# Kernel optimization log

Hardware: AMD Instinct MI355X
Metric: run time of the kernel (lower is better)

## Reference

```python
import jax, jax.numpy as jnp
import numpy as np

N_PATCHES = 16
HID = 8
HEADS = 2
DH = HID // HEADS          # 4
L = 2                       # n_blocks
DIM = 10                    # betas.shape[0]
C = 3
S_DIM = 224
PS = S_DIM // N_PATCHES     # 14
INPUT_D = C * PS * PS       # 588
SEQ = N_PATCHES ** 2 + 1    # 257
MLP = 4 * HID               # 32
EPS = 1e-5


def _pos_embed():
    i = np.arange(SEQ, dtype=np.float64)[:, None]
    j = np.arange(HID, dtype=np.float64)[None, :]
    ang = i / 10000.0 ** ((j - (j % 2)) / HID)
    pe = np.where(j % 2 == 0, np.sin(ang), np.cos(ang))
    return jnp.asarray(pe, jnp.float32)


def setup_inputs() -> dict:
    key = jax.random.key(0)
    ks = jax.random.split(key, 24)
    g = lambda k, shape: (jax.random.normal(k, shape, jnp.float32) * 0.1)
    inp = {
        'images': jax.random.normal(ks[0], (512, C, S_DIM, S_DIM), jnp.float32),
        'inputs_labels': jax.random.randint(ks[1], (512,), 0, C),
        'Wm': g(ks[2], (INPUT_D, HID)), 'bm': g(ks[3], (HID,)),
        'cls_table': g(ks[4], (C, HID)),
        'pe': _pos_embed(),
        'ln1_g': jnp.ones((L, HID)), 'ln1_b': jnp.zeros((L, HID)),
        'Wq': g(ks[5], (L, HEADS, DH, DH)), 'bq': g(ks[6], (L, HEADS, DH)),
        'Wk': g(ks[7], (L, HEADS, DH, DH)), 'bk': g(ks[8], (L, HEADS, DH)),
        'Wv': g(ks[9], (L, HEADS, DH, DH)), 'bv': g(ks[10], (L, HEADS, DH)),
        'ln2_g': jnp.ones((L, HID)), 'ln2_b': jnp.zeros((L, HID)),
        'W1': g(ks[11], (L, HID, MLP)), 'b1': g(ks[12], (L, MLP)),
        'W2': g(ks[13], (L, MLP, HID)), 'b2': g(ks[14], (L, HID)),
        'Wf': g(ks[15], (HID, DIM)), 'bf': g(ks[16], (DIM,)),
    }
    return inp


def _layernorm(x, g, b):
    m = jnp.mean(x, axis=-1, keepdims=True)
    v = jnp.mean(jnp.square(x - m), axis=-1, keepdims=True)
    return (x - m) * jax.lax.rsqrt(v + EPS) * g + b


def _forward(images, inputs_labels, Wm, bm, cls_table, pe,
             ln1_g, ln1_b, Wq, bq, Wk, bk, Wv, bv,
             ln2_g, ln2_b, W1, b1, W2, b2, Wf, bf):
    n = images.shape[0]
    # patchify: [n,C,H,W] -> [n, n_patches^2, C*ps*ps]
    p = images.reshape(n, C, N_PATCHES, PS, N_PATCHES, PS)
    p = p.transpose(0, 2, 4, 1, 3, 5).reshape(n, N_PATCHES ** 2, INPUT_D)
    tokens = p @ Wm + bm                                # [n, 256, HID]
    cls = cls_table[inputs_labels][:, None, :]          # [n, 1, HID]
    x = jnp.concatenate([cls, tokens], axis=1) + pe[None]  # [n, SEQ, HID]
    scale = 1.0 / jnp.sqrt(jnp.float32(DH))
    for l in range(L):
        h = _layernorm(x, ln1_g[l], ln1_b[l]).reshape(n, SEQ, HEADS, DH)
        q = jnp.einsum('nshd,hde->nhse', h, Wq[l]) + bq[l][None, :, None, :]
        k = jnp.einsum('nshd,hde->nhse', h, Wk[l]) + bk[l][None, :, None, :]
        v = jnp.einsum('nshd,hde->nhse', h, Wv[l]) + bv[l][None, :, None, :]
        att = jax.nn.softmax(jnp.einsum('nhse,nhte->nhst', q, k) * scale, axis=-1)
        o = jnp.einsum('nhst,nhte->nhse', att, v)       # [n,H,S,DH]
        x = x + o.transpose(0, 2, 1, 3).reshape(n, SEQ, HID)
        h2 = _layernorm(x, ln2_g[l], ln2_b[l])
        x = x + jax.nn.gelu(h2 @ W1[l] + b1[l], approximate=False) @ W2[l] + b2[l]
    return x[:, 0] @ Wf + bf                            # [n, DIM]


def reference(images, inputs_labels, Wm, bm, cls_table, pe,
              ln1_g, ln1_b, Wq, bq, Wk, bk, Wv, bv,
              ln2_g, ln2_b, W1, b1, W2, b2, Wf, bf):
    return _forward(images, inputs_labels, Wm, bm, cls_table, pe,
                    ln1_g, ln1_b, Wq, bq, Wk, bk, Wv, bv,
                    ln2_g, ln2_b, W1, b1, W2, b2, Wf, bf)
```

## Files before the change

kernel.cpp:

```cpp
#include <hip/hip_runtime.h>

#define N_IMG_D 150528
#define CH_STRIDE 50176

__global__ __launch_bounds__(256) void k_patch_embed(
    const float* __restrict__ img, const float* __restrict__ Wm,
    const float* __restrict__ bm, const float* __restrict__ pe,
    float* __restrict__ xws)
{
    __shared__ __align__(16) float wmA[588 * 4];
    __shared__ __align__(16) float wmB[588 * 4];
    __shared__ __align__(16) float red[224 * 8];

    const int t = threadIdx.x;
    const int b = blockIdx.x;
    const int n = b >> 4, py = b & 15;

    for (int i = t; i < 1176; i += 256) {
        float4 w = reinterpret_cast<const float4*>(Wm)[i];
        float* dst = (i & 1) ? wmB : wmA;
        *reinterpret_cast<float4*>(dst + (i >> 1) * 4) = w;
    }
    __syncthreads();

    if (t < 224) {
        const int rp = t / 112;
        const int t1 = t - rp * 112;
        const int px = t1 / 7;
        const int j  = t1 - px * 7;
        const int col0 = 2 * j;
        const float* ib = img + (size_t)n * N_IMG_D + (py * 14) * 224 + px * 14 + col0;
        float a0=0,a1=0,a2=0,a3=0,a4=0,a5=0,a6=0,a7=0;
        int c = 0, r = rp;
        const float* wA = wmA + (rp * 14 + col0) * 4;
        const float* wB = wmB + (rp * 14 + col0) * 4;
        #pragma unroll
        for (int it = 0; it < 21; ++it) {
            const float2 v = *reinterpret_cast<const float2*>(ib + c * CH_STRIDE + r * 224);
            const float4 wa0 = *reinterpret_cast<const float4*>(wA);
            const float4 wa1 = *reinterpret_cast<const float4*>(wA + 4);
            const float4 wb0 = *reinterpret_cast<const float4*>(wB);
            const float4 wb1 = *reinterpret_cast<const float4*>(wB + 4);
            a0 += v.x * wa0.x + v.y * wa1.x;
            a1 += v.x * wa0.y + v.y * wa1.y;
            a2 += v.x * wa0.z + v.y * wa1.z;
            a3 += v.x * wa0.w + v.y * wa1.w;
            a4 += v.x * wb0.x + v.y * wb1.x;
            a5 += v.x * wb0.y + v.y * wb1.y;
            a6 += v.x * wb0.z + v.y * wb1.z;
            a7 += v.x * wb0.w + v.y * wb1.w;
            r += 2;
            if (r >= 14) { r -= 14; c += 1; }
            wA += 28 * 4; wB += 28 * 4;
        }
        *reinterpret_cast<float4*>(red + t * 8)     = make_float4(a0, a1, a2, a3);
        *reinterpret_cast<float4*>(red + t * 8 + 4) = make_float4(a4, a5, a6, a7);
    }
    __syncthreads();

    if (t < 128) {
        const int px = t >> 3, e = t & 7;
        float s = 0.f;
        #pragma unroll
        for (int rp = 0; rp < 2; ++rp) {
            #pragma unroll
            for (int j = 0; j < 7; ++j)
                s += red[(rp * 112 + px * 7 + j) * 8 + e];
        }
        const int row = 1 + py * 16 + px;
        s += bm[e] + pe[row * 8 + e];
        xws[((size_t)n * 257 + row) * 8 + e] = s;
    }
}

__global__ __launch_bounds__(576) void k_transformer(
    const float* __restrict__ xws, const int* __restrict__ labels,
    const float* __restrict__ cls_table, const float* __restrict__ pe,
    const float* __restrict__ ln1_g, const float* __restrict__ ln1_b,
    const float* __restrict__ Wq, const float* __restrict__ bq,
    const float* __restrict__ Wk, const float* __restrict__ bk,
    const float* __restrict__ Wv, const float* __restrict__ bv,
    const float* __restrict__ ln2_g, const float* __restrict__ ln2_b,
    const float* __restrict__ W1, const float* __restrict__ b1,
    const float* __restrict__ W2, const float* __restrict__ b2,
    const float* __restrict__ Wf, const float* __restrict__ bf,
    float* __restrict__ out)
{
    __shared__ __align__(16) float xb[257 * 9];
    __shared__ __align__(16) float hb[257 * 9];
    __shared__ __align__(16) float kb[2 * 257 * 4];
    __shared__ __align__(16) float vb[2 * 257 * 4];
    __shared__ float wqs[64], wks[64], wvs[64];
    __shared__ float bqs[16], bks[16], bvs[16];
    __shared__ float w1s[512], b1s[64], w2s[512], b2s[16];

    const int t = threadIdx.x;
    const int n = blockIdx.x;
    const float* xn = xws + (size_t)n * 2056;

    for (int i = t; i < 64; i += 576) { wqs[i] = Wq[i]; wks[i] = Wk[i]; wvs[i] = Wv[i]; b1s[i] = b1[i]; }
    for (int i = t; i < 16; i += 576) { bqs[i] = bq[i]; bks[i] = bk[i]; bvs[i] = bv[i]; b2s[i] = b2[i]; }
    for (int i = t; i < 512; i += 576) { w1s[i] = W1[i]; w2s[i] = W2[i]; }

    if (t < 512) {
        float4 v = reinterpret_cast<const float4*>(xn)[t + 2];
        const int s = (t + 2) >> 1;
        const int e0 = (t & 1) ? 4 : 0;
        float* d = xb + s * 9 + e0;
        d[0] = v.x; d[1] = v.y; d[2] = v.z; d[3] = v.w;
    } else if (t < 520) {
        const int e = t - 512;
        xb[e] = cls_table[labels[n] * 8 + e] + pe[e];
    }
    __syncthreads();

    for (int l = 0; l < 2; ++l) {
        if (t < 257) {
            float v0[8]; float m = 0.f;
            #pragma unroll
            for (int e = 0; e < 8; ++e) { v0[e] = xb[t * 9 + e]; m += v0[e]; }
            m *= 0.125f;
            float var = 0.f;
            #pragma unroll
            for (int e = 0; e < 8; ++e) { float d = v0[e] - m; var += d * d; }
            var *= 0.125f;
            const float rs = rsqrtf(var + 1e-5f);
            const float* g = ln1_g + l * 8; const float* bb = ln1_b + l * 8;
            #pragma unroll
            for (int e = 0; e < 8; ++e) hb[t * 9 + e] = (v0[e] - m) * rs * g[e] + bb[e];
        }
        __syncthreads();

        if (t < 514) {
            const int h = (t >= 257) ? 1 : 0;
            const int s = t - 257 * h;
            float hv[4];
            #pragma unroll
            for (int d = 0; d < 4; ++d) hv[d] = hb[s * 9 + h * 4 + d];
            const float* wk = wks + (l * 2 + h) * 16; const float* bk_ = bks + (l * 2 + h) * 4;
            const float* wv = wvs + (l * 2 + h) * 16; const float* bv_ = bvs + (l * 2 + h) * 4;
            float kk[4], vv[4];
            #pragma unroll
            for (int e = 0; e < 4; ++e) { kk[e] = bk_[e]; vv[e] = bv_[e]; }
            #pragma unroll
            for (int d = 0; d < 4; ++d)
                #pragma unroll
                for (int e = 0; e < 4; ++e) {
                    kk[e] += hv[d] * wk[d * 4 + e];
                    vv[e] += hv[d] * wv[d * 4 + e];
                }
            *reinterpret_cast<float4*>(kb + (h * 257 + s) * 4) = make_float4(kk[0], kk[1], kk[2], kk[3]);
            *reinterpret_cast<float4*>(vb + (h * 257 + s) * 4) = make_float4(vv[0], vv[1], vv[2], vv[3]);
        }
        __syncthreads();

        if (t < 514) {
            const int h = (t >= 257) ? 1 : 0;
            const int s = t - 257 * h;
            float hv[4];
            #pragma unroll
            for (int d = 0; d < 4; ++d) hv[d] = hb[s * 9 + h * 4 + d];
            const float* wq = wqs + (l * 2 + h) * 16; const float* bq_ = bqs + (l * 2 + h) * 4;
            float q[4];
            #pragma unroll
            for (int e = 0; e < 4; ++e) q[e] = bq_[e];
            #pragma unroll
            for (int d = 0; d < 4; ++d)
                #pragma unroll
                for (int e = 0; e < 4; ++e) q[e] += hv[d] * wq[d * 4 + e];
            const float SC = 0.72134752044f;
            #pragma unroll
            for (int e = 0; e < 4; ++e) q[e] *= SC;

            const float4* kp = reinterpret_cast<const float4*>(kb) + h * 257;
            const float4* vp = reinterpret_cast<const float4*>(vb) + h * 257;
            float lsum = 0.f, o0 = 0.f, o1 = 0.f, o2 = 0.f, o3 = 0.f;
            #pragma unroll 4
            for (int tt = 0; tt < 257; ++tt) {
                const float4 kk = kp[tt];
                const float s2 = q[0] * kk.x + q[1] * kk.y + q[2] * kk.z + q[3] * kk.w;
                const float p = exp2f(s2);
                lsum += p;
                const float4 vv = vp[tt];
                o0 += p * vv.x; o1 += p * vv.y; o2 += p * vv.z; o3 += p * vv.w;
            }
            const float inv = 1.0f / lsum;
            float* xr = xb + s * 9 + h * 4;
            xr[0] += o0 * inv; xr[1] += o1 * inv; xr[2] += o2 * inv; xr[3] += o3 * inv;
        }
        __syncthreads();

        if (t < 257) {
            float v0[8]; float m = 0.f;
            #pragma unroll
            for (int e = 0; e < 8; ++e) { v0[e] = xb[t * 9 + e]; m += v0[e]; }
            m *= 0.125f;
            float var = 0.f;
            #pragma unroll
            for (int e = 0; e < 8; ++e) { float d = v0[e] - m; var += d * d; }
            var *= 0.125f;
            const float rs = rsqrtf(var + 1e-5f);
            const float* g = ln2_g + l * 8; const float* bb = ln2_b + l * 8;
            #pragma unroll
            for (int e = 0; e < 8; ++e) hb[t * 9 + e] = (v0[e] - m) * rs * g[e] + bb[e];
        }
        __syncthreads();

        if (t < 257) {
            float hv[8];
            #pragma unroll
            for (int e = 0; e < 8; ++e) hv[e] = hb[t * 9 + e];
            float acc[8] = {0.f, 0.f, 0.f, 0.f, 0.f, 0.f, 0.f, 0.f};
            const float* w1 = w1s + l * 256; const float* bb1 = b1s + l * 32;
            const float* w2 = w2s + l * 256; const float* bb2 = b2s + l * 8;
            for (int u = 0; u < 32; ++u) {
                float a = bb1[u];
                #pragma unroll
                for (int e = 0; e < 8; ++e) a += hv[e] * w1[e * 32 + u];
                const float gl = 0.5f * a * (1.0f + erff(a * 0.70710678f));
                #pragma unroll
                for (int e = 0; e < 8; ++e) acc[e] += gl * w2[u * 8 + e];
            }
            #pragma unroll
            for (int e = 0; e < 8; ++e) xb[t * 9 + e] += acc[e] + bb2[e];
        }
        __syncthreads();
    }

    if (t < 10) {
        float a = bf[t];
        #pragma unroll
        for (int e = 0; e < 8; ++e) a += xb[e] * Wf[e * 10 + t];
        out[(size_t)n * 10 + t] = a;
    }
}

extern "C" void kernel_launch(void* const* d_in, const int* in_sizes, int n_in,
                              void* d_out, int out_size, void* d_ws, size_t ws_size,
                              hipStream_t stream) {
    const float* img    = (const float*)d_in[0];
    const int*   labels = (const int*)  d_in[1];
    const float* Wm     = (const float*)d_in[2];
    const float* bm     = (const float*)d_in[3];
    const float* cls    = (const float*)d_in[4];
    const float* pe     = (const float*)d_in[5];
    const float* ln1_g  = (const float*)d_in[6];
    const float* ln1_b  = (const float*)d_in[7];
    const float* Wq     = (const float*)d_in[8];
    const float* bq     = (const float*)d_in[9];
    const float* Wk     = (const float*)d_in[10];
    const float* bk     = (const float*)d_in[11];
    const float* Wv     = (const float*)d_in[12];
    const float* bv     = (const float*)d_in[13];
    const float* ln2_g  = (const float*)d_in[14];
    const float* ln2_b  = (const float*)d_in[15];
    const float* W1     = (const float*)d_in[16];
    const float* b1     = (const float*)d_in[17];
    const float* W2     = (const float*)d_in[18];
    const float* b2     = (const float*)d_in[19];
    const float* Wf     = (const float*)d_in[20];
    const float* bf     = (const float*)d_in[21];
    float* out = (float*)d_out;
    float* xws = (float*)d_ws;

    const int n = in_sizes[0] / N_IMG_D;
    k_patch_embed<<<n * 16, 256, 0, stream>>>(img, Wm, bm, pe, xws);
    k_transformer<<<n, 576, 0, stream>>>(xws, labels, cls, pe, ln1_g, ln1_b,
        Wq, bq, Wk, bk, Wv, bv, ln2_g, ln2_b, W1, b1, W2, b2, Wf, bf, out);
}
```

Baseline: 538.6 us.

## Fuse LN1 with QKV projection and process two queries per attention thread

LayerNorm1 now computes Q, K and V for both heads directly in registers and writes them to shared memory. This removes the separate hb round trip and one barrier. The attention loop then gives each thread two query rows, so every K/V shared-memory load is reused twice, and only 258 threads are active instead of 514. In exchange, fewer waves run during attention, which is the dominant phase, so latency hiding may drop. A qb buffer is also added to shared memory.

```diff
diff --git a/kernel.cpp b/kernel.cpp
--- a/kernel.cpp
+++ b/kernel.cpp
@@ -88,6 +88,7 @@
 {
     __shared__ __align__(16) float xb[257 * 9];
     __shared__ __align__(16) float hb[257 * 9];
+    __shared__ __align__(16) float qb[2 * 257 * 4];
     __shared__ __align__(16) float kb[2 * 257 * 4];
     __shared__ __align__(16) float vb[2 * 257 * 4];
     __shared__ float wqs[64], wks[64], wvs[64];
@@ -114,6 +115,8 @@
     }
     __syncthreads();
 
+    const float SC = 0.72134752044f;
+
     for (int l = 0; l < 2; ++l) {
         if (t < 257) {
             float v0[8]; float m = 0.f;
@@ -126,67 +129,72 @@
             var *= 0.125f;
             const float rs = rsqrtf(var + 1e-5f);
             const float* g = ln1_g + l * 8; const float* bb = ln1_b + l * 8;
-            #pragma unroll
-            for (int e = 0; e < 8; ++e) hb[t * 9 + e] = (v0[e] - m) * rs * g[e] + bb[e];
-        }
-        __syncthreads();
-
-        if (t < 514) {
-            const int h = (t >= 257) ? 1 : 0;
-            const int s = t - 257 * h;
-            float hv[4];
-            #pragma unroll
-            for (int d = 0; d < 4; ++d) hv[d] = hb[s * 9 + h * 4 + d];
-            const float* wk = wks + (l * 2 + h) * 16; const float* bk_ = bks + (l * 2 + h) * 4;
-            const float* wv = wvs + (l * 2 + h) * 16; const float* bv_ = bvs + (l * 2 + h) * 4;
-            float kk[4], vv[4];
-            #pragma unroll
-            for (int e = 0; e < 4; ++e) { kk[e] = bk_[e]; vv[e] = bv_[e]; }
-            #pragma unroll
-            for (int d = 0; d < 4; ++d)
-                #pragma unroll
-                for (int e = 0; e < 4; ++e) {
-                    kk[e] += hv[d] * wk[d * 4 + e];
-                    vv[e] += hv[d] * wv[d * 4 + e];
+            float ln[8];
+            #pragma unroll
+            for (int e = 0; e < 8; ++e) ln[e] = (v0[e] - m) * rs * g[e] + bb[e];
+
+            #pragma unroll
+            for (int h = 0; h < 2; ++h) {
+                const int wb_ = (l * 2 + h);
+                const float* wq = wqs + wb_ * 16; const float* bq_ = bqs + wb_ * 4;
+                const float* wk = wks + wb_ * 16; const float* bk_ = bks + wb_ * 4;
+                const float* wv = wvs + wb_ * 16; const float* bv_ = bvs + wb_ * 4;
+                float qq[4], kk[4], vv[4];
+                #pragma unroll
+                for (int e = 0; e < 4; ++e) { qq[e] = bq_[e]; kk[e] = bk_[e]; vv[e] = bv_[e]; }
+                #pragma unroll
+                for (int d = 0; d < 4; ++d) {
+                    const float hd = ln[h * 4 + d];
+                    #pragma unroll
+                    for (int e = 0; e < 4; ++e) {
+                        qq[e] += hd * wq[d * 4 + e];
+                        kk[e] += hd * wk[d * 4 + e];
+                        vv[e] += hd * wv[d * 4 + e];
+                    }
                 }
-            *reinterpret_cast<float4*>(kb + (h * 257 + s) * 4) = make_float4(kk[0], kk[1], kk[2], kk[3]);
-            *reinterpret_cast<float4*>(vb + (h * 257 + s) * 4) = make_float4(vv[0], vv[1], vv[2], vv[3]);
-        }
-        __syncthreads();
-
-        if (t < 514) {
-            const int h = (t >= 257) ? 1 : 0;
-            const int s = t - 257 * h;
-            float hv[4];
-            #pragma unroll
-            for (int d = 0; d < 4; ++d) hv[d] = hb[s * 9 + h * 4 + d];
-            const float* wq = wqs + (l * 2 + h) * 16; const float* bq_ = bqs + (l * 2 + h) * 4;
-            float q[4];
-            #pragma unroll
-            for (int e = 0; e < 4; ++e) q[e] = bq_[e];
-            #pragma unroll
-            for (int d = 0; d < 4; ++d)
-                #pragma unroll
-                for (int e = 0; e < 4; ++e) q[e] += hv[d] * wq[d * 4 + e];
-            const float SC = 0.72134752044f;
-            #pragma unroll
-            for (int e = 0; e < 4; ++e) q[e] *= SC;
-
+                const int ri = (h * 257 + t) * 4;
+                *reinterpret_cast<float4*>(qb + ri) =
+                    make_float4(qq[0] * SC, qq[1] * SC, qq[2] * SC, qq[3] * SC);
+                *reinterpret_cast<float4*>(kb + ri) = make_float4(kk[0], kk[1], kk[2], kk[3]);
+                *reinterpret_cast<float4*>(vb + ri) = make_float4(vv[0], vv[1], vv[2], vv[3]);
+            }
+        }
+        __syncthreads();
+
+        if (t < 258) {
+            const int h = (t >= 129) ? 1 : 0;
+            const int j = t - 129 * h;
+            const int s0 = j;
+            const int s1 = j + 129;
+            const bool has2 = (j < 128);
+            const float4* qp = reinterpret_cast<const float4*>(qb) + h * 257;
             const float4* kp = reinterpret_cast<const float4*>(kb) + h * 257;
             const float4* vp = reinterpret_cast<const float4*>(vb) + h * 257;
-            float lsum = 0.f, o0 = 0.f, o1 = 0.f, o2 = 0.f, o3 = 0.f;
+            const float4 q0 = qp[s0];
+            const float4 q1 = qp[has2 ? s1 : s0];
+
+            float l0 = 0.f, o00 = 0.f, o01 = 0.f, o02 = 0.f, o03 = 0.f;
+            float l1 = 0.f, o10 = 0.f, o11 = 0.f, o12 = 0.f, o13 = 0.f;
             #pragma unroll 4
             for (int tt = 0; tt < 257; ++tt) {
                 const float4 kk = kp[tt];
-                const float s2 = q[0] * kk.x + q[1] * kk.y + q[2] * kk.z + q[3] * kk.w;
-                const float p = exp2f(s2);
-                lsum += p;
                 const float4 vv = vp[tt];
-                o0 += p * vv.x; o1 += p * vv.y; o2 += p * vv.z; o3 += p * vv.w;
-            }
-            const float inv = 1.0f / lsum;
-            float* xr = xb + s * 9 + h * 4;
-            xr[0] += o0 * inv; xr[1] += o1 * inv; xr[2] += o2 * inv; xr[3] += o3 * inv;
+                const float d0 = q0.x * kk.x + q0.y * kk.y + q0.z * kk.z + q0.w * kk.w;
+                const float d1 = q1.x * kk.x + q1.y * kk.y + q1.z * kk.z + q1.w * kk.w;
+                const float p0 = exp2f(d0);
+                const float p1 = exp2f(d1);
+                l0 += p0; l1 += p1;
+                o00 += p0 * vv.x; o01 += p0 * vv.y; o02 += p0 * vv.z; o03 += p0 * vv.w;
+                o10 += p1 * vv.x; o11 += p1 * vv.y; o12 += p1 * vv.z; o13 += p1 * vv.w;
+            }
+            const float i0 = 1.0f / l0;
+            float* xr0 = xb + s0 * 9 + h * 4;
+            xr0[0] += o00 * i0; xr0[1] += o01 * i0; xr0[2] += o02 * i0; xr0[3] += o03 * i0;
+            if (has2) {
+                const float i1 = 1.0f / l1;
+                float* xr1 = xb + s1 * 9 + h * 4;
+                xr1[0] += o10 * i1; xr1[1] += o11 * i1; xr1[2] += o12 * i1; xr1[3] += o13 * i1;
+            }
         }
         __syncthreads();
 
```

Measured after the change: 564.8 us. +4.9%, slower.
